# Kernel tuning notes

Hardware: AMD Instinct MI355X
Metric: run time of the kernel (lower is better)

## Reference

```python
import jax, jax.numpy as jnp
import numpy as np

N_NODES = 50000
N_GRAPHS = 512
HIDDEN = 128
BN_EPS = 1e-5


def setup_inputs() -> dict:
    key = jax.random.key(0)
    ks = jax.random.split(key, 16)
    E = 800000
    x = jax.random.normal(ks[0], (N_NODES, 1), dtype=jnp.float32)
    pos = jax.random.normal(ks[1], (N_NODES, 3), dtype=jnp.float32)
    edge_index = jax.random.randint(ks[2], (2, E), 0, N_NODES, dtype=jnp.int64)
    batch = jnp.sort(jax.random.randint(ks[3], (N_NODES,), 0, N_GRAPHS, dtype=jnp.int64))

    def lin(k, fan_in, fan_out):
        bound = 1.0 / np.sqrt(fan_in)
        return jax.random.uniform(k, (fan_in, fan_out), jnp.float32, -bound, bound)

    # conv1: in=1 -> concat dim 2*1+3=5
    c1_w1 = lin(ks[4], 5, HIDDEN); c1_b1 = jnp.zeros((HIDDEN,), jnp.float32)
    c1_w2 = lin(ks[5], HIDDEN, HIDDEN); c1_b2 = jnp.zeros((HIDDEN,), jnp.float32)
    # conv2: in=128 -> concat dim 2*128+3=259
    c2_w1 = lin(ks[6], 2 * HIDDEN + 3, HIDDEN); c2_b1 = jnp.zeros((HIDDEN,), jnp.float32)
    c2_w2 = lin(ks[7], HIDDEN, HIDDEN); c2_b2 = jnp.zeros((HIDDEN,), jnp.float32)
    # predictor MLP [128, 128, 1], bias=[False, True], batch_norm + relu between
    p_w1 = lin(ks[8], HIDDEN, HIDDEN)
    bn_gamma = jnp.ones((HIDDEN,), jnp.float32)
    bn_beta = jnp.zeros((HIDDEN,), jnp.float32)
    p_w2 = lin(ks[9], HIDDEN, 1)
    p_b2 = jnp.zeros((1,), jnp.float32)
    return {
        "x": x, "pos": pos, "edge_index": edge_index, "batch": batch,
        "c1_w1": c1_w1, "c1_b1": c1_b1, "c1_w2": c1_w2, "c1_b2": c1_b2,
        "c2_w1": c2_w1, "c2_b1": c2_b1, "c2_w2": c2_w2, "c2_b2": c2_b2,
        "p_w1": p_w1, "bn_gamma": bn_gamma, "bn_beta": bn_beta,
        "p_w2": p_w2, "p_b2": p_b2,
    }


def _conv(x, pos, src, dst, w1, b1, w2, b2):
    # gather endpoints; PyG: x_j = x[src], x_i = x[dst], aggregate into dst
    feat = jnp.concatenate([x[dst], x[src], pos[src] - pos[dst]], axis=-1)  # [E, 2F+3]
    msg = jax.nn.relu(feat @ w1 + b1) @ w2 + b2  # [E, H]
    return jax.ops.segment_sum(msg, dst, num_segments=N_NODES)  # [N, H]


def reference(x, pos, edge_index, batch,
              c1_w1, c1_b1, c1_w2, c1_b2,
              c2_w1, c2_b1, c2_w2, c2_b2,
              p_w1, bn_gamma, bn_beta, p_w2, p_b2):
    src, dst = edge_index[0], edge_index[1]
    h = jax.nn.relu(_conv(x, pos, src, dst, c1_w1, c1_b1, c1_w2, c1_b2))
    h = jax.nn.relu(_conv(h, pos, src, dst, c2_w1, c2_b1, c2_w2, c2_b2))
    g = jax.ops.segment_sum(h, batch, num_segments=N_GRAPHS)  # [G, H] global add pool
    # predictor: Linear(no bias) -> BatchNorm(train stats) -> ReLU -> Linear(bias)
    z = g @ p_w1
    mean = jnp.mean(z, axis=0)
    var = jnp.var(z, axis=0)
    z = bn_gamma * (z - mean) * jax.lax.rsqrt(var + BN_EPS) + bn_beta
    z = jax.nn.relu(z)
    return z @ p_w2 + p_b2  # [G, 1]
```

## Files before the change

### kernel.cpp

```cpp
#include <hip/hip_runtime.h>
#include <hip/hip_bf16.h>

#define HID 128
#define DMAX 64
#define DSTRIDE 32

typedef unsigned int uint;
typedef unsigned short ushort;
using short8 = __attribute__((ext_vector_type(8))) short;
using f32x4  = __attribute__((ext_vector_type(4))) float;

#define MFMA_B16(a, b, c) __builtin_amdgcn_mfma_f32_16x16x32_bf16(a, b, c, 0, 0, 0)

__device__ inline ushort bf16rn(float f) {
  uint u = __float_as_uint(f);
  u += 0x7fff + ((u >> 16) & 1);
  return (ushort)(u >> 16);
}
__device__ inline uint packbf(float a, float b) {
  return (uint)bf16rn(a) | ((uint)bf16rn(b) << 16);
}
__device__ inline float bflo(uint u) { return __uint_as_float(u << 16); }
__device__ inline float bfhi(uint u) { return __uint_as_float(u & 0xffff0000u); }

__global__ __launch_bounds__(256) void k_prep(
    const float* __restrict__ x, const float* __restrict__ pos,
    const float* __restrict__ c1w2, const float* __restrict__ c2w1, const float* __restrict__ c2w2,
    float4* __restrict__ xp, int* __restrict__ degP, float* __restrict__ g,
    ushort* __restrict__ w1t, ushort* __restrict__ wdt,
    ushort* __restrict__ wst, ushort* __restrict__ w2t,
    int N, int G, int Npad) {
  int idx = blockIdx.x * 256 + threadIdx.x;
  int stride = gridDim.x * 256;
  for (int i = idx; i < Npad * DSTRIDE; i += stride) degP[i] = 0;
  if (idx < G * HID) g[idx] = 0.f;
  if (idx < N) {
    xp[idx] = make_float4(pos[3 * idx], pos[3 * idx + 1], pos[3 * idx + 2], x[idx]);
  }
  {
    int m = idx >> 14, e = idx & 16383;
    int c = e >> 7, k = e & 127;
    const float* src;
    ushort* dst;
    if (m == 0)      { src = c1w2;              dst = w1t; }
    else if (m == 1) { src = c2w1;              dst = wdt; }
    else if (m == 2) { src = c2w1 + 128 * 128;  dst = wst; }
    else             { src = c2w2;              dst = w2t; }
    dst[e] = bf16rn(src[k * 128 + c]);
  }
}

__global__ void k_build(const int* __restrict__ dstv, const int* __restrict__ srcv,
                        int* __restrict__ degP, int* __restrict__ srcsP, int E) {
  int e = blockIdx.x * 256 + threadIdx.x;
  if (e < E) {
    int d = dstv[e];
    int r = atomicAdd(&degP[(size_t)d * DSTRIDE], 1);
    if (r < DMAX) srcsP[(size_t)d * DMAX + r] = srcv[e];
  }
}

__global__ __launch_bounds__(64) void k_conv1(
    const float4* __restrict__ xp,
    const int* __restrict__ degP, const int* __restrict__ srcsP,
    const float* __restrict__ w1, const float* __restrict__ b1, uint* __restrict__ hs) {
  int n = blockIdx.x;
  int lane = threadIdx.x;
  int f0 = 2 * lane;
  __shared__ float sxs[64];
  __shared__ float sdp[3][64];
  int cnt = min(degP[(size_t)n * DSTRIDE], DMAX);
  float4 me = xp[n];
  float xi = me.w;
  float2 a1 = *(const float2*)&w1[HID + f0];
  float2 a2 = *(const float2*)&w1[2 * HID + f0];
  float2 a3 = *(const float2*)&w1[3 * HID + f0];
  float2 a4 = *(const float2*)&w1[4 * HID + f0];
  float c_0 = fmaf(xi, w1[f0],     b1[f0]);
  float c_1 = fmaf(xi, w1[f0 + 1], b1[f0 + 1]);
  float acc0 = 0.f, acc1 = 0.f;
  if (lane < cnt) {
    int s = srcsP[(size_t)n * DMAX + lane];
    float4 v = xp[s];
    sxs[lane] = v.w;
    sdp[0][lane] = v.x - me.x;
    sdp[1][lane] = v.y - me.y;
    sdp[2][lane] = v.z - me.z;
  }
  __syncthreads();
  for (int k = 0; k < cnt; ++k) {
    float xj = sxs[k], d0 = sdp[0][k], d1 = sdp[1][k], d2 = sdp[2][k];
    float h0 = fmaf(xj, a1.x, fmaf(d0, a2.x, fmaf(d1, a3.x, fmaf(d2, a4.x, c_0))));
    float h1 = fmaf(xj, a1.y, fmaf(d0, a2.y, fmaf(d1, a3.y, fmaf(d2, a4.y, c_1))));
    acc0 += fmaxf(h0, 0.f);
    acc1 += fmaxf(h1, 0.f);
  }
  hs[(size_t)n * 64 + lane] = packbf(acc0, acc1);
}

__global__ __launch_bounds__(512) void k_mfuse(
    const ushort* __restrict__ A, const ushort* __restrict__ W1t,
    const ushort* __restrict__ Wdt, const ushort* __restrict__ Wst,
    const float* __restrict__ b1, const float* __restrict__ bd,
    const int* __restrict__ degP,
    uint* __restrict__ psb, uint* __restrict__ pdb, int M) {
  __shared__ uint hl[64][68];
  __shared__ uint hd[64][68];
  int t = threadIdx.x;
  int l = t & 63;
  int rl = l & 15, kg = l >> 4;
  int wv = t >> 6;
  int rg = wv & 3;
  int cg = wv >> 2;
  int rloc = rg * 16 + rl;
  int r = blockIdx.x * 64 + rloc;
  int rc = min(r, M - 1);
  bool valid = (r < M);
  const short8* arow = (const short8*)(A + (size_t)rc * 128);
  short8 af0 = arow[kg], af1 = arow[4 + kg], af2 = arow[8 + kg], af3 = arow[12 + kg];
  float dg = valid ? (float)degP[(size_t)r * DSTRIDE] : 0.f;
  #pragma unroll
  for (int ntl = 0; ntl < 4; ++ntl) {
    int nt = cg * 4 + ntl;
    const short8* wrow = (const short8*)(W1t + (size_t)(nt * 16 + rl) * 128);
    f32x4 acc = {0.f, 0.f, 0.f, 0.f};
    acc = MFMA_B16(wrow[kg],      af0, acc);
    acc = MFMA_B16(wrow[4 + kg],  af1, acc);
    acc = MFMA_B16(wrow[8 + kg],  af2, acc);
    acc = MFMA_B16(wrow[12 + kg], af3, acc);
    int c0 = nt * 16 + kg * 4;
    f32x4 b4 = *(const f32x4*)&b1[c0];
    float v0 = fmaxf(fmaf(dg, b4[0], acc[0]), 0.f);
    float v1 = fmaxf(fmaf(dg, b4[1], acc[1]), 0.f);
    float v2 = fmaxf(fmaf(dg, b4[2], acc[2]), 0.f);
    float v3 = fmaxf(fmaf(dg, b4[3], acc[3]), 0.f);
    hl[rloc][(c0 >> 1)]     = packbf(v0, v1);
    hl[rloc][(c0 >> 1) + 1] = packbf(v2, v3);
  }
  __syncthreads();
  const uint* hrow = hl[rloc];
  short8 bfrag[4];
  #pragma unroll
  for (int i = 0; i < 4; ++i) bfrag[i] = *(const short8*)&hrow[i * 16 + kg * 4];
  __syncthreads();
  #pragma unroll
  for (int ntl = 0; ntl < 4; ++ntl) {
    int nt = cg * 4 + ntl;
    const short8* wsrow = (const short8*)(Wst + (size_t)(nt * 16 + rl) * 128);
    const short8* wdrow = (const short8*)(Wdt + (size_t)(nt * 16 + rl) * 128);
    f32x4 accS = {0.f, 0.f, 0.f, 0.f};
    f32x4 accD = {0.f, 0.f, 0.f, 0.f};
    accS = MFMA_B16(wsrow[kg],      bfrag[0], accS);
    accS = MFMA_B16(wsrow[4 + kg],  bfrag[1], accS);
    accS = MFMA_B16(wsrow[8 + kg],  bfrag[2], accS);
    accS = MFMA_B16(wsrow[12 + kg], bfrag[3], accS);
    accD = MFMA_B16(wdrow[kg],      bfrag[0], accD);
    accD = MFMA_B16(wdrow[4 + kg],  bfrag[1], accD);
    accD = MFMA_B16(wdrow[8 + kg],  bfrag[2], accD);
    accD = MFMA_B16(wdrow[12 + kg], bfrag[3], accD);
    int c0 = nt * 16 + kg * 4;
    f32x4 b4 = *(const f32x4*)&bd[c0];
    hl[rloc][(c0 >> 1)]     = packbf(accS[0], accS[1]);
    hl[rloc][(c0 >> 1) + 1] = packbf(accS[2], accS[3]);
    hd[rloc][(c0 >> 1)]     = packbf(accD[0] + b4[0], accD[1] + b4[1]);
    hd[rloc][(c0 >> 1) + 1] = packbf(accD[2] + b4[2], accD[3] + b4[3]);
  }
  __syncthreads();
  int rbase = blockIdx.x * 64;
  #pragma unroll
  for (int idx = t; idx < 64 * 16; idx += 512) {
    int row = idx >> 4, c4 = (idx & 15) * 4;
    int gr = rbase + row;
    if (gr < M) {
      *(uint4*)&psb[(size_t)gr * 64 + c4] = *(const uint4*)&hl[row][c4];
      *(uint4*)&pdb[(size_t)gr * 64 + c4] = *(const uint4*)&hd[row][c4];
    }
  }
}

__global__ __launch_bounds__(64) void k_conv2(
    const float4* __restrict__ xp,
    const int* __restrict__ degP, const int* __restrict__ srcsP,
    const uint* __restrict__ pdb, const uint* __restrict__ ps,
    const float* __restrict__ wc, uint* __restrict__ hs) {
  int n = blockIdx.x;
  int lane = threadIdx.x;
  int eg = lane >> 4;
  int fb = lane & 15;
  int f0 = 8 * fb;
  __shared__ int ssrc[64];
  __shared__ float sdp[3][64];
  int cnt = min(degP[(size_t)n * DSTRIDE], DMAX);
  float4 me = xp[n];
  float c0[8], c1[8], c2[8], pdv[8], acc[8];
  uint4 pdu = *(const uint4*)&pdb[(size_t)n * 64 + fb * 4];
  uint pdua[4] = {pdu.x, pdu.y, pdu.z, pdu.w};
  #pragma unroll
  for (int i = 0; i < 4; ++i) {
    pdv[2 * i]     = bflo(pdua[i]);
    pdv[2 * i + 1] = bfhi(pdua[i]);
  }
  #pragma unroll
  for (int i = 0; i < 8; ++i) {
    c0[i]  = wc[f0 + i];
    c1[i]  = wc[HID + f0 + i];
    c2[i]  = wc[2 * HID + f0 + i];
    acc[i] = 0.f;
  }
  if (lane < cnt) {
    int s = srcsP[(size_t)n * DMAX + lane];
    float4 v = xp[s];
    ssrc[lane] = s;
    sdp[0][lane] = v.x - me.x;
    sdp[1][lane] = v.y - me.y;
    sdp[2][lane] = v.z - me.z;
  }
  __syncthreads();
  for (int k = 0; k < cnt; k += 16) {
    int ke[4] = {k + eg, k + 4 + eg, k + 8 + eg, k + 12 + eg};
    int kc[4];
    #pragma unroll
    for (int j = 0; j < 4; ++j) kc[j] = min(ke[j], cnt - 1);
    int se[4] = {ssrc[kc[0]], ssrc[kc[1]], ssrc[kc[2]], ssrc[kc[3]]};
    uint4 u[4];
    #pragma unroll
    for (int j = 0; j < 4; ++j) u[j] = *(const uint4*)&ps[(size_t)se[j] * 64 + fb * 4];
    #pragma unroll
    for (int j = 0; j < 4; ++j) {
      float dd0 = sdp[0][kc[j]], dd1 = sdp[1][kc[j]], dd2 = sdp[2][kc[j]];
      bool vv = ke[j] < cnt;
      uint uu[4] = {u[j].x, u[j].y, u[j].z, u[j].w};
      if (vv) {
        #pragma unroll
        for (int q = 0; q < 4; ++q) {
          float w0  = pdv[2*q]   + fmaf(dd0, c0[2*q],   fmaf(dd1, c1[2*q],   dd2 * c2[2*q]));
          float w1v = pdv[2*q+1] + fmaf(dd0, c0[2*q+1], fmaf(dd1, c1[2*q+1], dd2 * c2[2*q+1]));
          acc[2*q]   += fmaxf(w0  + bflo(uu[q]), 0.f);
          acc[2*q+1] += fmaxf(w1v + bfhi(uu[q]), 0.f);
        }
      }
    }
  }
  #pragma unroll
  for (int i = 0; i < 8; ++i) {
    acc[i] += __shfl_xor(acc[i], 16);
    acc[i] += __shfl_xor(acc[i], 32);
  }
  if (eg == 0) {
    uint4 o;
    o.x = packbf(acc[0], acc[1]);
    o.y = packbf(acc[2], acc[3]);
    o.z = packbf(acc[4], acc[5]);
    o.w = packbf(acc[6], acc[7]);
    *(uint4*)&hs[(size_t)n * 64 + fb * 4] = o;
  }
}

__global__ __launch_bounds__(256) void k_mpool(
    const ushort* __restrict__ A, const ushort* __restrict__ Wt,
    const float* __restrict__ bias, const int* __restrict__ degP, const int* __restrict__ batch,
    float* __restrict__ Of, int M) {
  int t = threadIdx.x;
  int l = t & 63;
  int rl = l & 15, kg = l >> 4;
  int r = blockIdx.x * 64 + (t >> 6) * 16 + rl;
  int rc = min(r, M - 1);
  bool valid = (r < M);
  const short8* arow = (const short8*)(A + (size_t)rc * 128);
  short8 af0 = arow[kg], af1 = arow[4 + kg], af2 = arow[8 + kg], af3 = arow[12 + kg];
  float dg = valid ? (float)degP[(size_t)r * DSTRIDE] : 0.f;
  int bt = batch[rc];
  int gf = __shfl(bt, 0);
  int gl = __shfl(bt, 15);
  #pragma unroll
  for (int nt = 0; nt < 8; ++nt) {
    const short8* wrow = (const short8*)(Wt + (size_t)(nt * 16 + rl) * 128);
    f32x4 acc = {0.f, 0.f, 0.f, 0.f};
    acc = MFMA_B16(wrow[kg],      af0, acc);
    acc = MFMA_B16(wrow[4 + kg],  af1, acc);
    acc = MFMA_B16(wrow[8 + kg],  af2, acc);
    acc = MFMA_B16(wrow[12 + kg], af3, acc);
    int c0 = nt * 16 + kg * 4;
    f32x4 b4 = *(const f32x4*)&bias[c0];
    float v0 = valid ? fmaxf(fmaf(dg, b4[0], acc[0]), 0.f) : 0.f;
    float v1 = valid ? fmaxf(fmaf(dg, b4[1], acc[1]), 0.f) : 0.f;
    float v2 = valid ? fmaxf(fmaf(dg, b4[2], acc[2]), 0.f) : 0.f;
    float v3 = valid ? fmaxf(fmaf(dg, b4[3], acc[3]), 0.f) : 0.f;
    for (int gg = gf; gg <= gl; ++gg) {
      bool mine = (bt == gg);
      float s0 = mine ? v0 : 0.f;
      float s1 = mine ? v1 : 0.f;
      float s2 = mine ? v2 : 0.f;
      float s3 = mine ? v3 : 0.f;
      #pragma unroll
      for (int m = 1; m <= 8; m <<= 1) {
        s0 += __shfl_xor(s0, m);
        s1 += __shfl_xor(s1, m);
        s2 += __shfl_xor(s2, m);
        s3 += __shfl_xor(s3, m);
      }
      if (rl == 0) {
        float* gp = &Of[(size_t)gg * 128 + c0];
        atomicAdd(gp + 0, s0);
        atomicAdd(gp + 1, s1);
        atomicAdd(gp + 2, s2);
        atomicAdd(gp + 3, s3);
      }
    }
  }
}

__global__ __launch_bounds__(256) void k_pgemm(
    const float* __restrict__ A, const float* __restrict__ W, float* __restrict__ O1, int M) {
  __shared__ float As[128][36];
  int t = threadIdx.x;
  int n0 = blockIdx.x * 32;
  int j = t & 127, m = t >> 7;
  for (int idx = t; idx < 32 * 128; idx += 256) {
    int r = idx >> 7, i = idx & 127;
    int n = n0 + r;
    As[i][r] = (n < M) ? A[(size_t)n * 128 + i] : 0.f;
  }
  __syncthreads();
  float acc[16];
  #pragma unroll
  for (int r = 0; r < 16; ++r) acc[r] = 0.f;
  int rb = m * 16;
  for (int i = 0; i < 128; ++i) {
    float w = W[i * 128 + j];
    const float4* ap = reinterpret_cast<const float4*>(&As[i][rb]);
    #pragma unroll
    for (int q = 0; q < 4; ++q) {
      float4 a = ap[q];
      acc[q * 4 + 0] = fmaf(a.x, w, acc[q * 4 + 0]);
      acc[q * 4 + 1] = fmaf(a.y, w, acc[q * 4 + 1]);
      acc[q * 4 + 2] = fmaf(a.z, w, acc[q * 4 + 2]);
      acc[q * 4 + 3] = fmaf(a.w, w, acc[q * 4 + 3]);
    }
  }
  #pragma unroll
  for (int r = 0; r < 16; ++r) {
    int n = n0 + rb + r;
    if (n < M) O1[(size_t)n * 128 + j] = acc[r];
  }
}

__global__ __launch_bounds__(256) void k_bn2(const float* __restrict__ z,
                                             float* __restrict__ mv, int G) {
  int j = blockIdx.x;
  int t = threadIdx.x;
  float v1 = (t < G) ? z[(size_t)t * 128 + j] : 0.f;
  float v2 = (t + 256 < G) ? z[(size_t)(t + 256) * 128 + j] : 0.f;
  float s = v1 + v2;
  float q = fmaf(v1, v1, v2 * v2);
  #pragma unroll
  for (int off = 32; off; off >>= 1) {
    s += __shfl_down(s, off);
    q += __shfl_down(q, off);
  }
  __shared__ float ws[4], wq[4];
  int wid = t >> 6, lane = t & 63;
  if (lane == 0) { ws[wid] = s; wq[wid] = q; }
  __syncthreads();
  if (t == 0) {
    float S = ws[0] + ws[1] + ws[2] + ws[3];
    float Q = wq[0] + wq[1] + wq[2] + wq[3];
    float mean = S / (float)G;
    float var = Q / (float)G - mean * mean;
    mv[j] = mean;
    mv[128 + j] = rsqrtf(var + 1e-5f);
  }
}

__global__ __launch_bounds__(256) void k_final(
    const float* __restrict__ z, const float* __restrict__ mv,
    const float* __restrict__ gamma, const float* __restrict__ beta,
    const float* __restrict__ w2, const float* __restrict__ b2,
    float* __restrict__ out, int G) {
  int wid = threadIdx.x >> 6, lane = threadIdx.x & 63;
  int r = blockIdx.x * 4 + wid;
  if (r >= G) return;
  float acc = 0.f;
  #pragma unroll
  for (int h = 0; h < 2; ++h) {
    int jj = lane + h * 64;
    float v = z[(size_t)r * 128 + jj];
    float zn = fmaf((v - mv[jj]) * mv[128 + jj], gamma[jj], beta[jj]);
    acc = fmaf(fmaxf(zn, 0.f), w2[jj], acc);
  }
  #pragma unroll
  for (int off = 32; off; off >>= 1) acc += __shfl_down(acc, off);
  if (lane == 0) out[r] = acc + b2[0];
}

extern "C" void kernel_launch(void* const* d_in, const int* in_sizes, int n_in,
                              void* d_out, int out_size, void* d_ws, size_t ws_size,
                              hipStream_t stream) {
  const float* x     = (const float*)d_in[0];
  const float* pos   = (const float*)d_in[1];
  const int*   eidx  = (const int*)d_in[2];
  const int*   batch = (const int*)d_in[3];
  const float* c1w1  = (const float*)d_in[4];
  const float* c1b1  = (const float*)d_in[5];
  const float* c1w2  = (const float*)d_in[6];
  const float* c1b2  = (const float*)d_in[7];
  const float* c2w1  = (const float*)d_in[8];
  const float* c2b1  = (const float*)d_in[9];
  const float* c2w2  = (const float*)d_in[10];
  const float* c2b2  = (const float*)d_in[11];
  const float* pw1   = (const float*)d_in[12];
  const float* gamma = (const float*)d_in[13];
  const float* beta  = (const float*)d_in[14];
  const float* pw2   = (const float*)d_in[15];
  const float* pb2   = (const float*)d_in[16];
  (void)n_in; (void)ws_size;

  const int N = in_sizes[0];
  const int E = in_sizes[2] / 2;
  const int G = out_size;
  const int* srcv = eidx;
  const int* dstv = eidx + E;

  char* w = (char*)d_ws;
  size_t o = 0;
  auto carve = [&](size_t bytes) { void* p = w + o; o = (o + bytes + 255) & ~(size_t)255; return p; };
  int Npad = ((N + 255) / 256) * 256;
  int* degP   = (int*)carve((size_t)Npad * DSTRIDE * 4);
  int* srcsP  = (int*)carve((size_t)N * DMAX * 4);
  float4* xp  = (float4*)carve((size_t)N * 16);
  uint*   hs1  = (uint*)carve((size_t)N * 64 * 4);
  uint*   pdb  = (uint*)carve((size_t)N * 64 * 4);
  uint*   psb  = (uint*)carve((size_t)N * 64 * 4);
  uint*   hs2  = (uint*)carve((size_t)N * 64 * 4);
  ushort* w1t  = (ushort*)carve(16384 * 2);
  ushort* wdt  = (ushort*)carve(16384 * 2);
  ushort* wst  = (ushort*)carve(16384 * 2);
  ushort* w2t  = (ushort*)carve(16384 * 2);
  float* g    = (float*)carve((size_t)G * HID * 4);
  float* z    = (float*)carve((size_t)G * HID * 4);
  float* mv   = (float*)carve(256 * 4);

  int nbE = (E + 255) / 256;

  k_prep<<<256, 256, 0, stream>>>(x, pos, c1w2, c2w1, c2w2,
                                  xp, degP, g, w1t, wdt, wst, w2t, N, G, Npad);
  k_build<<<nbE, 256, 0, stream>>>(dstv, srcv, degP, srcsP, E);

  int gb = (N + 63) / 64;
  k_conv1<<<N, 64, 0, stream>>>(xp, degP, srcsP, c1w1, c1b1, hs1);
  k_mfuse<<<gb, 512, 0, stream>>>((const ushort*)hs1, w1t, wdt, wst, c1b2, c2b1, degP,
                                  psb, pdb, N);
  k_conv2<<<N, 64, 0, stream>>>(xp, degP, srcsP, pdb, psb, c2w1 + 256 * HID, hs2);
  k_mpool<<<gb, 256, 0, stream>>>((const ushort*)hs2, w2t, c2b2, degP, batch, g, N);
  k_pgemm<<<(G + 31) / 32, 256, 0, stream>>>(g, pw1, z, G);
  k_bn2<<<HID, 256, 0, stream>>>(z, mv, G);
  k_final<<<(G + 3) / 4, 256, 0, stream>>>(z, mv, gamma, beta, pw2, pb2, (float*)d_out, G);
}
```

Measured before the change: 205.8 us.

## Compact degree array, process two edges per thread, fuse BN stats into pgemm

The degree counters were padded to one per 128-byte stride. They are now stored densely, which shrinks the zeroing pass in k_prep from Npad*32 ints to Npad ints. k_build handles two edges per thread with int2 loads. The separate BN statistics kernel is removed: k_pgemm accumulates per-column sums and sums of squares with atomics into mv, and k_final computes the mean and rstd inline, saving one launch. The trade-off is more atomic contention on the dense degree counters, a variance formula computed from sums, and float atomics whose order is nondeterministic.

```diff
diff --git a/kernel.cpp b/kernel.cpp
--- a/kernel.cpp
+++ b/kernel.cpp
@@ -3,7 +3,6 @@
 
 #define HID 128
 #define DMAX 64
-#define DSTRIDE 32
 
 typedef unsigned int uint;
 typedef unsigned short ushort;
@@ -26,14 +25,15 @@
 __global__ __launch_bounds__(256) void k_prep(
     const float* __restrict__ x, const float* __restrict__ pos,
     const float* __restrict__ c1w2, const float* __restrict__ c2w1, const float* __restrict__ c2w2,
-    float4* __restrict__ xp, int* __restrict__ degP, float* __restrict__ g,
+    float4* __restrict__ xp, int* __restrict__ deg, float* __restrict__ g,
+    float* __restrict__ mv,
     ushort* __restrict__ w1t, ushort* __restrict__ wdt,
     ushort* __restrict__ wst, ushort* __restrict__ w2t,
     int N, int G, int Npad) {
   int idx = blockIdx.x * 256 + threadIdx.x;
-  int stride = gridDim.x * 256;
-  for (int i = idx; i < Npad * DSTRIDE; i += stride) degP[i] = 0;
+  if (idx < Npad) deg[idx] = 0;
   if (idx < G * HID) g[idx] = 0.f;
+  if (idx < 256) mv[idx] = 0.f;
   if (idx < N) {
     xp[idx] = make_float4(pos[3 * idx], pos[3 * idx + 1], pos[3 * idx + 2], x[idx]);
   }
@@ -51,25 +51,33 @@
 }
 
 __global__ void k_build(const int* __restrict__ dstv, const int* __restrict__ srcv,
-                        int* __restrict__ degP, int* __restrict__ srcsP, int E) {
-  int e = blockIdx.x * 256 + threadIdx.x;
-  if (e < E) {
-    int d = dstv[e];
-    int r = atomicAdd(&degP[(size_t)d * DSTRIDE], 1);
-    if (r < DMAX) srcsP[(size_t)d * DMAX + r] = srcv[e];
+                        int* __restrict__ deg, int* __restrict__ srcsP, int E) {
+  int i = blockIdx.x * 256 + threadIdx.x;
+  int e0 = 2 * i;
+  if (e0 + 1 < E) {
+    int2 d2 = *(const int2*)&dstv[e0];
+    int2 s2 = *(const int2*)&srcv[e0];
+    int r0 = atomicAdd(&deg[d2.x], 1);
+    int r1 = atomicAdd(&deg[d2.y], 1);
+    if (r0 < DMAX) srcsP[(size_t)d2.x * DMAX + r0] = s2.x;
+    if (r1 < DMAX) srcsP[(size_t)d2.y * DMAX + r1] = s2.y;
+  } else if (e0 < E) {
+    int d = dstv[e0];
+    int r = atomicAdd(&deg[d], 1);
+    if (r < DMAX) srcsP[(size_t)d * DMAX + r] = srcv[e0];
   }
 }
 
 __global__ __launch_bounds__(64) void k_conv1(
     const float4* __restrict__ xp,
-    const int* __restrict__ degP, const int* __restrict__ srcsP,
+    const int* __restrict__ deg, const int* __restrict__ srcsP,
     const float* __restrict__ w1, const float* __restrict__ b1, uint* __restrict__ hs) {
   int n = blockIdx.x;
   int lane = threadIdx.x;
   int f0 = 2 * lane;
   __shared__ float sxs[64];
   __shared__ float sdp[3][64];
-  int cnt = min(degP[(size_t)n * DSTRIDE], DMAX);
+  int cnt = min(deg[n], DMAX);
   float4 me = xp[n];
   float xi = me.w;
   float2 a1 = *(const float2*)&w1[HID + f0];
@@ -102,7 +110,7 @@
     const ushort* __restrict__ A, const ushort* __restrict__ W1t,
     const ushort* __restrict__ Wdt, const ushort* __restrict__ Wst,
     const float* __restrict__ b1, const float* __restrict__ bd,
-    const int* __restrict__ degP,
+    const int* __restrict__ deg,
     uint* __restrict__ psb, uint* __restrict__ pdb, int M) {
   __shared__ uint hl[64][68];
   __shared__ uint hd[64][68];
@@ -118,7 +126,7 @@
   bool valid = (r < M);
   const short8* arow = (const short8*)(A + (size_t)rc * 128);
   short8 af0 = arow[kg], af1 = arow[4 + kg], af2 = arow[8 + kg], af3 = arow[12 + kg];
-  float dg = valid ? (float)degP[(size_t)r * DSTRIDE] : 0.f;
+  float dg = valid ? (float)deg[r] : 0.f;
   #pragma unroll
   for (int ntl = 0; ntl < 4; ++ntl) {
     int nt = cg * 4 + ntl;
@@ -180,7 +188,7 @@
 
 __global__ __launch_bounds__(64) void k_conv2(
     const float4* __restrict__ xp,
-    const int* __restrict__ degP, const int* __restrict__ srcsP,
+    const int* __restrict__ deg, const int* __restrict__ srcsP,
     const uint* __restrict__ pdb, const uint* __restrict__ ps,
     const float* __restrict__ wc, uint* __restrict__ hs) {
   int n = blockIdx.x;
@@ -190,7 +198,7 @@
   int f0 = 8 * fb;
   __shared__ int ssrc[64];
   __shared__ float sdp[3][64];
-  int cnt = min(degP[(size_t)n * DSTRIDE], DMAX);
+  int cnt = min(deg[n], DMAX);
   float4 me = xp[n];
   float c0[8], c1[8], c2[8], pdv[8], acc[8];
   uint4 pdu = *(const uint4*)&pdb[(size_t)n * 64 + fb * 4];
@@ -258,7 +266,7 @@
 
 __global__ __launch_bounds__(256) void k_mpool(
     const ushort* __restrict__ A, const ushort* __restrict__ Wt,
-    const float* __restrict__ bias, const int* __restrict__ degP, const int* __restrict__ batch,
+    const float* __restrict__ bias, const int* __restrict__ deg, const int* __restrict__ batch,
     float* __restrict__ Of, int M) {
   int t = threadIdx.x;
   int l = t & 63;
@@ -268,7 +276,7 @@
   bool valid = (r < M);
   const short8* arow = (const short8*)(A + (size_t)rc * 128);
   short8 af0 = arow[kg], af1 = arow[4 + kg], af2 = arow[8 + kg], af3 = arow[12 + kg];
-  float dg = valid ? (float)degP[(size_t)r * DSTRIDE] : 0.f;
+  float dg = valid ? (float)deg[r] : 0.f;
   int bt = batch[rc];
   int gf = __shfl(bt, 0);
   int gl = __shfl(bt, 15);
@@ -311,7 +319,8 @@
 }
 
 __global__ __launch_bounds__(256) void k_pgemm(
-    const float* __restrict__ A, const float* __restrict__ W, float* __restrict__ O1, int M) {
+    const float* __restrict__ A, const float* __restrict__ W, float* __restrict__ O1,
+    float* __restrict__ mv, int M) {
   __shared__ float As[128][36];
   int t = threadIdx.x;
   int n0 = blockIdx.x * 32;
@@ -338,38 +347,18 @@
       acc[q * 4 + 3] = fmaf(a.w, w, acc[q * 4 + 3]);
     }
   }
+  float S = 0.f, Q = 0.f;
   #pragma unroll
   for (int r = 0; r < 16; ++r) {
     int n = n0 + rb + r;
-    if (n < M) O1[(size_t)n * 128 + j] = acc[r];
-  }
-}
-
-__global__ __launch_bounds__(256) void k_bn2(const float* __restrict__ z,
-                                             float* __restrict__ mv, int G) {
-  int j = blockIdx.x;
-  int t = threadIdx.x;
-  float v1 = (t < G) ? z[(size_t)t * 128 + j] : 0.f;
-  float v2 = (t + 256 < G) ? z[(size_t)(t + 256) * 128 + j] : 0.f;
-  float s = v1 + v2;
-  float q = fmaf(v1, v1, v2 * v2);
-  #pragma unroll
-  for (int off = 32; off; off >>= 1) {
-    s += __shfl_down(s, off);
-    q += __shfl_down(q, off);
-  }
-  __shared__ float ws[4], wq[4];
-  int wid = t >> 6, lane = t & 63;
-  if (lane == 0) { ws[wid] = s; wq[wid] = q; }
-  __syncthreads();
-  if (t == 0) {
-    float S = ws[0] + ws[1] + ws[2] + ws[3];
-    float Q = wq[0] + wq[1] + wq[2] + wq[3];
-    float mean = S / (float)G;
-    float var = Q / (float)G - mean * mean;
-    mv[j] = mean;
-    mv[128 + j] = rsqrtf(var + 1e-5f);
-  }
+    if (n < M) {
+      O1[(size_t)n * 128 + j] = acc[r];
+      S += acc[r];
+      Q = fmaf(acc[r], acc[r], Q);
+    }
+  }
+  atomicAdd(&mv[j], S);
+  atomicAdd(&mv[128 + j], Q);
 }
 
 __global__ __launch_bounds__(256) void k_final(
@@ -381,11 +370,15 @@
   int r = blockIdx.x * 4 + wid;
   if (r >= G) return;
   float acc = 0.f;
+  float invG = 1.f / (float)G;
   #pragma unroll
   for (int h = 0; h < 2; ++h) {
     int jj = lane + h * 64;
+    float mean = mv[jj] * invG;
+    float var = mv[128 + jj] * invG - mean * mean;
+    float rstd = rsqrtf(var + 1e-5f);
     float v = z[(size_t)r * 128 + jj];
-    float zn = fmaf((v - mv[jj]) * mv[128 + jj], gamma[jj], beta[jj]);
+    float zn = fmaf((v - mean) * rstd, gamma[jj], beta[jj]);
     acc = fmaf(fmaxf(zn, 0.f), w2[jj], acc);
   }
   #pragma unroll
@@ -425,7 +418,7 @@
   size_t o = 0;
   auto carve = [&](size_t bytes) { void* p = w + o; o = (o + bytes + 255) & ~(size_t)255; return p; };
   int Npad = ((N + 255) / 256) * 256;
-  int* degP   = (int*)carve((size_t)Npad * DSTRIDE * 4);
+  int* deg    = (int*)carve((size_t)Npad * 4);
   int* srcsP  = (int*)carve((size_t)N * DMAX * 4);
   float4* xp  = (float4*)carve((size_t)N * 16);
   uint*   hs1  = (uint*)carve((size_t)N * 64 * 4);
@@ -440,19 +433,17 @@
   float* z    = (float*)carve((size_t)G * HID * 4);
   float* mv   = (float*)carve(256 * 4);
 
-  int nbE = (E + 255) / 256;
-
   k_prep<<<256, 256, 0, stream>>>(x, pos, c1w2, c2w1, c2w2,
-                                  xp, degP, g, w1t, wdt, wst, w2t, N, G, Npad);
-  k_build<<<nbE, 256, 0, stream>>>(dstv, srcv, degP, srcsP, E);
+                                  xp, deg, g, mv, w1t, wdt, wst, w2t, N, G, Npad);
+  int nbB = ((E + 1) / 2 + 255) / 256;
+  k_build<<<nbB, 256, 0, stream>>>(dstv, srcv, deg, srcsP, E);
 
   int gb = (N + 63) / 64;
-  k_conv1<<<N, 64, 0, stream>>>(xp, degP, srcsP, c1w1, c1b1, hs1);
-  k_mfuse<<<gb, 512, 0, stream>>>((const ushort*)hs1, w1t, wdt, wst, c1b2, c2b1, degP,
+  k_conv1<<<N, 64, 0, stream>>>(xp, deg, srcsP, c1w1, c1b1, hs1);
+  k_mfuse<<<gb, 512, 0, stream>>>((const ushort*)hs1, w1t, wdt, wst, c1b2, c2b1, deg,
                                   psb, pdb, N);
-  k_conv2<<<N, 64, 0, stream>>>(xp, degP, srcsP, pdb, psb, c2w1 + 256 * HID, hs2);
-  k_mpool<<<gb, 256, 0, stream>>>((const ushort*)hs2, w2t, c2b2, degP, batch, g, N);
-  k_pgemm<<<(G + 31) / 32, 256, 0, stream>>>(g, pw1, z, G);
-  k_bn2<<<HID, 256, 0, stream>>>(z, mv, G);
+  k_conv2<<<N, 64, 0, stream>>>(xp, deg, srcsP, pdb, psb, c2w1 + 256 * HID, hs2);
+  k_mpool<<<gb, 256, 0, stream>>>((const ushort*)hs2, w2t, c2b2, deg, batch, g, N);
+  k_pgemm<<<(G + 31) / 32, 256, 0, stream>>>(g, pw1, z, mv, G);
   k_final<<<(G + 3) / 4, 256, 0, stream>>>(z, mv, gamma, beta, pw2, pb2, (float*)d_out, G);
 }
```

Measured after the change: 198.6 us. 1.04x faster.
